# Kernel optimization log

Hardware: AMD Instinct MI355X
Metric: run time of the kernel (lower is better)

## Reference

```python
import jax, jax.numpy as jnp
import numpy as np
from jax import lax

# DCNv2 (ModulatedDeformConvPack) constants per init_kwargs
STRIDE, PAD, DIL, DG, KH, KW = 1, 1, 1, 1, 3, 3
K = KH * KW


def setup_inputs() -> dict:
    key = jax.random.key(0)
    k0, k1, k2 = jax.random.split(key, 3)
    B, C, H, W = 2, 64, 128, 128
    O = 64
    x = jax.random.normal(k0, (B, C, H, W), jnp.float32)
    weight = jax.random.normal(k1, (O, C, KH, KW), jnp.float32) / np.sqrt(C * KH * KW)
    bias = jnp.zeros((O,), jnp.float32)
    # small scale so predicted offsets stay within a few pixels (realistic trained DCN)
    offset_w = jax.random.normal(k2, (DG * 3 * K, C, KH, KW), jnp.float32) * 0.01
    offset_b = jnp.zeros((DG * 3 * K,), jnp.float32)
    return {"x": x, "weight": weight, "bias": bias, "offset_w": offset_w, "offset_b": offset_b}


def _modulated_deform_conv(x, weight, bias, offset_w, offset_b):
    B, C, H, W = x.shape
    O = weight.shape[0]
    # 1) offset/mask prediction conv (standard conv, same geometry as main conv)
    off = lax.conv_general_dilated(
        x, offset_w, window_strides=(STRIDE, STRIDE), padding=((PAD, PAD), (PAD, PAD)),
        rhs_dilation=(DIL, DIL), dimension_numbers=("NCHW", "OIHW", "NCHW"))
    off = off + offset_b[None, :, None, None]
    Ho, Wo = off.shape[2], off.shape[3]
    o1, o2, m = jnp.split(off, 3, axis=1)
    dy = o1.reshape(B, DG, K, Ho, Wo)
    dx = o2.reshape(B, DG, K, Ho, Wo)
    mask = jax.nn.sigmoid(m).reshape(B, DG, K, Ho, Wo)

    # 2) sampling positions: p = p0 + k*dil - pad + offset
    ki, kj = jnp.meshgrid(jnp.arange(KH), jnp.arange(KW), indexing="ij")
    base_y = (jnp.arange(Ho) * STRIDE - PAD)[None, :, None] + (ki.reshape(K) * DIL)[:, None, None]  # (K,Ho,1)
    base_x = (jnp.arange(Wo) * STRIDE - PAD)[None, None, :] + (kj.reshape(K) * DIL)[:, None, None]  # (K,1,Wo)
    py = base_y[None, None].astype(x.dtype) + dy  # (B,DG,K,Ho,Wo)
    px = base_x[None, None].astype(x.dtype) + dx

    y0 = jnp.floor(py)
    x0 = jnp.floor(px)
    wy = py - y0  # fractional weights
    wx = px - x0
    y0i = y0.astype(jnp.int32)
    x0i = x0.astype(jnp.int32)

    Cg = C // DG
    xg = x.reshape(B, DG, Cg, H * W)

    def corner(yi, xi):
        valid = ((yi >= 0) & (yi < H) & (xi >= 0) & (xi < W)).astype(x.dtype)  # zero-pad outside
        idx = jnp.clip(yi, 0, H - 1) * W + jnp.clip(xi, 0, W - 1)  # (B,DG,K,Ho,Wo)
        gather = lambda xf, id_: xf[:, id_]  # (Cg, K, Ho, Wo)
        vals = jax.vmap(jax.vmap(gather))(xg, idx)  # (B,DG,Cg,K,Ho,Wo)
        return vals * valid[:, :, None]

    wy_ = wy[:, :, None]
    wx_ = wx[:, :, None]
    samp = (corner(y0i, x0i) * (1 - wy_) * (1 - wx_)
            + corner(y0i, x0i + 1) * (1 - wy_) * wx_
            + corner(y0i + 1, x0i) * wy_ * (1 - wx_)
            + corner(y0i + 1, x0i + 1) * wy_ * wx_)
    samp = samp * mask[:, :, None]  # modulation
    samp = samp.reshape(B, C, K, Ho, Wo)

    # 3) contraction with conv weight (groups=1)
    out = jnp.einsum("bckhw,ock->bohw", samp, weight.reshape(O, C, K))
    return out + bias[None, :, None, None]


def reference(x, weight, bias, offset_w, offset_b):
    return _modulated_deform_conv(x, weight, bias, offset_w, offset_b)
```

## Files before the change

kernel.cpp:

```cpp
#include <hip/hip_runtime.h>
#include <hip/hip_bf16.h>

typedef __attribute__((ext_vector_type(8))) short bf16x8;
typedef __attribute__((ext_vector_type(4))) float f32x4;

#define Bc 2
#define Cc 64
#define Hc 128
#define Wc 128
#define Oc 64
#define NOFF 27
#define HWc (Hc * Wc)

__device__ __forceinline__ short f2bf(float f) {
    __hip_bfloat16 h = __float2bfloat16(f);
    return __builtin_bit_cast(short, h);
}
__device__ __forceinline__ float bf2f(short s) {
    __hip_bfloat16 h = __builtin_bit_cast(__hip_bfloat16, s);
    return __bfloat162float(h);
}

__global__ __launch_bounds__(256) void prep_kernel(
    const float* __restrict__ x, const float* __restrict__ w, const float* __restrict__ ow,
    short* __restrict__ xT, short* __restrict__ Ahi, short* __restrict__ Alo,
    short* __restrict__ Ohi, short* __restrict__ Olo) {
    int bid = blockIdx.x;
    int t = threadIdx.x;
    if (bid < 512) {
        int b = bid >> 8, rem = bid & 255;
        int h = rem >> 1, w0 = (rem & 1) << 6;
        __shared__ float tile[64][68];
        {
            int c = t >> 2, sub = t & 3;
            const float* src = x + ((size_t)(b * Cc + c) * Hc + h) * Wc + w0 + sub * 16;
#pragma unroll
            for (int j = 0; j < 4; ++j)
                *(float4*)&tile[c][sub * 16 + 4 * j] = *(const float4*)(src + 4 * j);
        }
        __syncthreads();
        {
            int ww = t >> 2, cs = (t & 3) << 4;
            short* dst = xT + (((size_t)(b * Hc + h)) * Wc + w0 + ww) * Cc + cs;
            bf16x8 v0, v1;
#pragma unroll
            for (int j = 0; j < 8; ++j) {
                v0[j] = f2bf(tile[cs + j][ww]);
                v1[j] = f2bf(tile[cs + 8 + j][ww]);
            }
            *(bf16x8*)(dst) = v0;
            *(bf16x8*)(dst + 8) = v1;
        }
    } else {
        int idx = (bid - 512) * 256 + t;
        const int NM = 4 * 18 * 64 * 8;
        const int NO = 2 * 18 * 64 * 8;
        if (idx < NM) {
            int j = idx & 7, lane = (idx >> 3) & 63, ks = (idx >> 9) % 18, mt = idx / 9216;
            int o  = mt * 16 + (lane & 15);
            int kk = ks >> 1;
            int c  = (ks & 1) * 32 + (lane >> 4) * 8 + j;
            float v = w[(o * Cc + c) * 9 + kk];
            short hi = f2bf(v);
            short lo = f2bf(v - bf2f(hi));
            Ahi[idx] = hi; Alo[idx] = lo;
        } else if (idx < NM + NO) {
            int t2 = idx - NM;
            int j = t2 & 7, lane = (t2 >> 3) & 63, ks = (t2 >> 9) % 18, mt = t2 / 9216;
            int o  = mt * 16 + (lane & 15);
            int kk = ks >> 1;
            int c  = (ks & 1) * 32 + (lane >> 4) * 8 + j;
            float v = (o < NOFF) ? ow[(o * Cc + c) * 9 + kk] : 0.f;
            short hi = f2bf(v);
            short lo = f2bf(v - bf2f(hi));
            Ohi[t2] = hi; Olo[t2] = lo;
        }
    }
}

__global__ __launch_bounds__(256, 2) void fused_dcn_kernel(
    const short* __restrict__ xT,
    const short* __restrict__ Ahi, const short* __restrict__ Alo,
    const short* __restrict__ Ohi, const short* __restrict__ Olo,
    const float* __restrict__ bias, const float* __restrict__ obias,
    float* __restrict__ out) {
    int bid = blockIdx.x;
    int b = bid >> 8, rem = bid & 255;
    int h = rem >> 1, w0 = (rem & 1) << 6;
    int tid = threadIdx.x;
    int lane = tid & 63, wv = tid >> 6;
    int n_loc = lane & 15, quad = lane >> 4;
    int p_glob = wv * 16 + n_loc;
    int wpix = w0 + p_glob;
    int cb0 = quad * 8;
    int cb1 = 32 + quad * 8;

    __shared__ float4 wgt[576];
    __shared__ int4   sidx[576];
    __shared__ float  tmp[NOFF * 64];

    const short* xb = xT + (size_t)b * HWc * Cc;

    f32x4 oacc0 = {0.f, 0.f, 0.f, 0.f}, oacc1 = {0.f, 0.f, 0.f, 0.f};
    bf16x8 s1A[2], s1B[2];
    {
        int yc = min(max(h - 1, 0), Hc - 1);
        int xc = min(max(wpix - 1, 0), Wc - 1);
        const short* base = xb + ((size_t)yc * Wc + xc) * Cc;
        s1A[0] = *(const bf16x8*)(base + cb0);
        s1A[1] = *(const bf16x8*)(base + cb1);
    }
#pragma unroll
    for (int kk = 0; kk < 9; ++kk) {
        bf16x8* cur = (kk & 1) ? s1B : s1A;
        bf16x8* nxt = (kk & 1) ? s1A : s1B;
        if (kk < 8) {
            int kk2 = kk + 1;
            int yc = min(max(h + kk2 / 3 - 1, 0), Hc - 1);
            int xc = min(max(wpix + kk2 % 3 - 1, 0), Wc - 1);
            const short* base = xb + ((size_t)yc * Wc + xc) * Cc;
            nxt[0] = *(const bf16x8*)(base + cb0);
            nxt[1] = *(const bf16x8*)(base + cb1);
        }
        int y = h + kk / 3 - 1, xw = wpix + kk % 3 - 1;
        bool val = ((unsigned)y < (unsigned)Hc) && ((unsigned)xw < (unsigned)Wc);
        bf16x8 z = {0, 0, 0, 0, 0, 0, 0, 0};
        bf16x8 b0 = val ? cur[0] : z;
        bf16x8 b1 = val ? cur[1] : z;
#pragma unroll
        for (int ks = 0; ks < 2; ++ks) {
            bf16x8 bf = ks ? b1 : b0;
            int ksg = kk * 2 + ks;
            bf16x8 ah0 = *(const bf16x8*)(Ohi + ((0 * 18 + ksg) * 64 + lane) * 8);
            bf16x8 al0 = *(const bf16x8*)(Olo + ((0 * 18 + ksg) * 64 + lane) * 8);
            oacc0 = __builtin_amdgcn_mfma_f32_16x16x32_bf16(ah0, bf, oacc0, 0, 0, 0);
            oacc0 = __builtin_amdgcn_mfma_f32_16x16x32_bf16(al0, bf, oacc0, 0, 0, 0);
            bf16x8 ah1 = *(const bf16x8*)(Ohi + ((1 * 18 + ksg) * 64 + lane) * 8);
            bf16x8 al1 = *(const bf16x8*)(Olo + ((1 * 18 + ksg) * 64 + lane) * 8);
            oacc1 = __builtin_amdgcn_mfma_f32_16x16x32_bf16(ah1, bf, oacc1, 0, 0, 0);
            oacc1 = __builtin_amdgcn_mfma_f32_16x16x32_bf16(al1, bf, oacc1, 0, 0, 0);
        }
    }
    {
        int mrow = quad * 4;
#pragma unroll
        for (int r = 0; r < 4; ++r) {
            int oc = mrow + r;
            if (oc < NOFF) tmp[oc * 64 + p_glob] = oacc0[r] + obias[oc];
            int oc2 = 16 + mrow + r;
            if (oc2 < NOFF) tmp[oc2 * 64 + p_glob] = oacc1[r] + obias[oc2];
        }
    }
    __syncthreads();

    for (int t = tid; t < 576; t += 256) {
        int k = t >> 6, p = t & 63;
        float dy = tmp[k * 64 + p];
        float dx = tmp[(9 + k) * 64 + p];
        float mm = tmp[(18 + k) * 64 + p];
        float m  = 1.f / (1.f + __expf(-mm));
        float py = (float)(h - 1 + k / 3) + dy;
        float px = (float)(w0 + p - 1 + k % 3) + dx;
        float y0f = floorf(py), x0f = floorf(px);
        float fy = py - y0f, fx = px - x0f;
        int y0 = (int)y0f, x0i = (int)x0f;
        float vy0 = (y0 >= 0 && y0 < Hc) ? 1.f : 0.f;
        float vy1 = (y0 + 1 >= 0 && y0 + 1 < Hc) ? 1.f : 0.f;
        float vx0 = (x0i >= 0 && x0i < Wc) ? 1.f : 0.f;
        float vx1 = (x0i + 1 >= 0 && x0i + 1 < Wc) ? 1.f : 0.f;
        wgt[t] = make_float4((1.f - fy) * (1.f - fx) * m * vy0 * vx0,
                             (1.f - fy) * fx         * m * vy0 * vx1,
                             fy         * (1.f - fx) * m * vy1 * vx0,
                             fy         * fx         * m * vy1 * vx1);
        int cy0 = min(max(y0, 0), Hc - 1) * Wc;
        int cy1 = min(max(y0 + 1, 0), Hc - 1) * Wc;
        int cx0 = min(max(x0i, 0), Wc - 1);
        int cx1 = min(max(x0i + 1, 0), Wc - 1);
        sidx[t] = make_int4(cy0 + cx0, cy0 + cx1, cy1 + cx0, cy1 + cx1);
    }
    __syncthreads();

    f32x4 acc[4] = {{0.f, 0.f, 0.f, 0.f}, {0.f, 0.f, 0.f, 0.f},
                    {0.f, 0.f, 0.f, 0.f}, {0.f, 0.f, 0.f, 0.f}};
    bf16x8 bufA[8], bufB[8];
    float4 w4 = wgt[p_glob];
    {
        int4 id = sidx[p_glob];
        const short* c00 = xb + (size_t)id.x * Cc;
        const short* c01 = xb + (size_t)id.y * Cc;
        const short* c10 = xb + (size_t)id.z * Cc;
        const short* c11 = xb + (size_t)id.w * Cc;
        bufA[0] = *(const bf16x8*)(c00 + cb0); bufA[1] = *(const bf16x8*)(c00 + cb1);
        bufA[2] = *(const bf16x8*)(c01 + cb0); bufA[3] = *(const bf16x8*)(c01 + cb1);
        bufA[4] = *(const bf16x8*)(c10 + cb0); bufA[5] = *(const bf16x8*)(c10 + cb1);
        bufA[6] = *(const bf16x8*)(c11 + cb0); bufA[7] = *(const bf16x8*)(c11 + cb1);
    }
#pragma unroll
    for (int kk = 0; kk < 9; ++kk) {
        bf16x8* cur = (kk & 1) ? bufB : bufA;
        bf16x8* nxt = (kk & 1) ? bufA : bufB;
        float4 w4n;
        if (kk < 8) {
            int4 idn = sidx[(kk + 1) * 64 + p_glob];
            w4n = wgt[(kk + 1) * 64 + p_glob];
            const short* c00 = xb + (size_t)idn.x * Cc;
            const short* c01 = xb + (size_t)idn.y * Cc;
            const short* c10 = xb + (size_t)idn.z * Cc;
            const short* c11 = xb + (size_t)idn.w * Cc;
            nxt[0] = *(const bf16x8*)(c00 + cb0); nxt[1] = *(const bf16x8*)(c00 + cb1);
            nxt[2] = *(const bf16x8*)(c01 + cb0); nxt[3] = *(const bf16x8*)(c01 + cb1);
            nxt[4] = *(const bf16x8*)(c10 + cb0); nxt[5] = *(const bf16x8*)(c10 + cb1);
            nxt[6] = *(const bf16x8*)(c11 + cb0); nxt[7] = *(const bf16x8*)(c11 + cb1);
        }
        bf16x8 b0, b1;
#pragma unroll
        for (int j = 0; j < 8; ++j) {
            float s0 = w4.x * bf2f(cur[0][j]) + w4.y * bf2f(cur[2][j])
                     + w4.z * bf2f(cur[4][j]) + w4.w * bf2f(cur[6][j]);
            float s1 = w4.x * bf2f(cur[1][j]) + w4.y * bf2f(cur[3][j])
                     + w4.z * bf2f(cur[5][j]) + w4.w * bf2f(cur[7][j]);
            b0[j] = f2bf(s0);
            b1[j] = f2bf(s1);
        }
#pragma unroll
        for (int ks = 0; ks < 2; ++ks) {
            bf16x8 bf = ks ? b1 : b0;
            int ksg = kk * 2 + ks;
#pragma unroll
            for (int mt = 0; mt < 4; ++mt) {
                bf16x8 ah = *(const bf16x8*)(Ahi + ((mt * 18 + ksg) * 64 + lane) * 8);
                bf16x8 al = *(const bf16x8*)(Alo + ((mt * 18 + ksg) * 64 + lane) * 8);
                acc[mt] = __builtin_amdgcn_mfma_f32_16x16x32_bf16(ah, bf, acc[mt], 0, 0, 0);
                acc[mt] = __builtin_amdgcn_mfma_f32_16x16x32_bf16(al, bf, acc[mt], 0, 0, 0);
            }
        }
        w4 = w4n;
    }

    int mrow = quad * 4;
    float* ob = out + ((size_t)b * Oc * Hc + h) * Wc + w0 + p_glob;
#pragma unroll
    for (int mt = 0; mt < 4; ++mt)
#pragma unroll
        for (int r = 0; r < 4; ++r) {
            int o = mt * 16 + mrow + r;
            ob[(size_t)o * HWc] = acc[mt][r] + bias[o];
        }
}

extern "C" void kernel_launch(void* const* d_in, const int* in_sizes, int n_in,
                              void* d_out, int out_size, void* d_ws, size_t ws_size,
                              hipStream_t stream) {
    const float* x        = (const float*)d_in[0];
    const float* weight   = (const float*)d_in[1];
    const float* bias     = (const float*)d_in[2];
    const float* offset_w = (const float*)d_in[3];
    const float* offset_b = (const float*)d_in[4];
    float* out = (float*)d_out;

    char* ws = (char*)d_ws;
    short* xT  = (short*)(ws + 0);
    short* Ahi = (short*)(ws + 4194304);
    short* Alo = (short*)(ws + 4268032);
    short* Ohi = (short*)(ws + 4341760);
    short* Olo = (short*)(ws + 4378624);

    prep_kernel<<<512 + 216, 256, 0, stream>>>(x, weight, offset_w, xT, Ahi, Alo, Ohi, Olo);
    fused_dcn_kernel<<<Bc * Hc * 2, 256, 0, stream>>>(xT, Ahi, Alo, Ohi, Olo, bias, offset_b, out);
}
```

Baseline: 105.2 us.

## Fuse prep and DCN kernels into one launch with inter-block flag sync

```diff
diff --git a/kernel.cpp b/kernel.cpp
--- a/kernel.cpp
+++ b/kernel.cpp
@@ -11,6 +11,7 @@
 #define Oc 64
 #define NOFF 27
 #define HWc (Hc * Wc)
+#define MAGIC 0x13579BDF
 
 __device__ __forceinline__ short f2bf(float f) {
     __hip_bfloat16 h = __float2bfloat16(f);
@@ -21,68 +22,19 @@
     return __bfloat162float(h);
 }
 
-__global__ __launch_bounds__(256) void prep_kernel(
+__device__ __forceinline__ void spin_on(volatile int* f) {
+    while (__hip_atomic_load((const int*)f, __ATOMIC_RELAXED, __HIP_MEMORY_SCOPE_AGENT) != MAGIC) {}
+}
+__device__ __forceinline__ void publish(int* f) {
+    __hip_atomic_store(f, MAGIC, __ATOMIC_RELAXED, __HIP_MEMORY_SCOPE_AGENT);
+}
+
+__global__ __launch_bounds__(256, 2) void mega_dcn_kernel(
     const float* __restrict__ x, const float* __restrict__ w, const float* __restrict__ ow,
+    const float* __restrict__ bias, const float* __restrict__ obias,
     short* __restrict__ xT, short* __restrict__ Ahi, short* __restrict__ Alo,
-    short* __restrict__ Ohi, short* __restrict__ Olo) {
-    int bid = blockIdx.x;
-    int t = threadIdx.x;
-    if (bid < 512) {
-        int b = bid >> 8, rem = bid & 255;
-        int h = rem >> 1, w0 = (rem & 1) << 6;
-        __shared__ float tile[64][68];
-        {
-            int c = t >> 2, sub = t & 3;
-            const float* src = x + ((size_t)(b * Cc + c) * Hc + h) * Wc + w0 + sub * 16;
-#pragma unroll
-            for (int j = 0; j < 4; ++j)
-                *(float4*)&tile[c][sub * 16 + 4 * j] = *(const float4*)(src + 4 * j);
-        }
-        __syncthreads();
-        {
-            int ww = t >> 2, cs = (t & 3) << 4;
-            short* dst = xT + (((size_t)(b * Hc + h)) * Wc + w0 + ww) * Cc + cs;
-            bf16x8 v0, v1;
-#pragma unroll
-            for (int j = 0; j < 8; ++j) {
-                v0[j] = f2bf(tile[cs + j][ww]);
-                v1[j] = f2bf(tile[cs + 8 + j][ww]);
-            }
-            *(bf16x8*)(dst) = v0;
-            *(bf16x8*)(dst + 8) = v1;
-        }
-    } else {
-        int idx = (bid - 512) * 256 + t;
-        const int NM = 4 * 18 * 64 * 8;
-        const int NO = 2 * 18 * 64 * 8;
-        if (idx < NM) {
-            int j = idx & 7, lane = (idx >> 3) & 63, ks = (idx >> 9) % 18, mt = idx / 9216;
-            int o  = mt * 16 + (lane & 15);
-            int kk = ks >> 1;
-            int c  = (ks & 1) * 32 + (lane >> 4) * 8 + j;
-            float v = w[(o * Cc + c) * 9 + kk];
-            short hi = f2bf(v);
-            short lo = f2bf(v - bf2f(hi));
-            Ahi[idx] = hi; Alo[idx] = lo;
-        } else if (idx < NM + NO) {
-            int t2 = idx - NM;
-            int j = t2 & 7, lane = (t2 >> 3) & 63, ks = (t2 >> 9) % 18, mt = t2 / 9216;
-            int o  = mt * 16 + (lane & 15);
-            int kk = ks >> 1;
-            int c  = (ks & 1) * 32 + (lane >> 4) * 8 + j;
-            float v = (o < NOFF) ? ow[(o * Cc + c) * 9 + kk] : 0.f;
-            short hi = f2bf(v);
-            short lo = f2bf(v - bf2f(hi));
-            Ohi[t2] = hi; Olo[t2] = lo;
-        }
-    }
-}
-
-__global__ __launch_bounds__(256, 2) void fused_dcn_kernel(
-    const short* __restrict__ xT,
-    const short* __restrict__ Ahi, const short* __restrict__ Alo,
-    const short* __restrict__ Ohi, const short* __restrict__ Olo,
-    const float* __restrict__ bias, const float* __restrict__ obias,
+    short* __restrict__ Ohi, short* __restrict__ Olo,
+    int* __restrict__ xflag, int* __restrict__ pflag,
     float* __restrict__ out) {
     int bid = blockIdx.x;
     int b = bid >> 8, rem = bid & 255;
@@ -92,12 +44,71 @@
     int n_loc = lane & 15, quad = lane >> 4;
     int p_glob = wv * 16 + n_loc;
     int wpix = w0 + p_glob;
-    int cb0 = quad * 8;
-    int cb1 = 32 + quad * 8;
-
+    int cb0 = quad * 8, cb1 = 32 + quad * 8;
+
+    __shared__ float tile[64][68];
     __shared__ float4 wgt[576];
     __shared__ int4   sidx[576];
     __shared__ float  tmp[NOFF * 64];
+    __shared__ int    rowmin, rowmax;
+
+    bool packO = (bid >= 144 && bid < 216);
+    if (packO) {
+        int idx = bid * 256 + tid;
+        int t2 = idx - 144 * 256;
+        int j = t2 & 7, ln = (t2 >> 3) & 63, ks = (t2 >> 9) % 18, mt = t2 / 9216;
+        int o = mt * 16 + (ln & 15);
+        int kk = ks >> 1;
+        int c = (ks & 1) * 32 + (ln >> 4) * 8 + j;
+        float v = (o < NOFF) ? ow[(o * Cc + c) * 9 + kk] : 0.f;
+        short hi = f2bf(v);
+        Ohi[t2] = hi; Olo[t2] = f2bf(v - bf2f(hi));
+        __syncthreads();
+        if (tid == 0) { __threadfence(); publish(&pflag[bid]); }
+    }
+    {
+        int c = tid >> 2, sub = tid & 3;
+        const float* src = x + ((size_t)(b * Cc + c) * Hc + h) * Wc + w0 + sub * 16;
+#pragma unroll
+        for (int j = 0; j < 4; ++j)
+            *(float4*)&tile[c][sub * 16 + 4 * j] = *(const float4*)(src + 4 * j);
+        __syncthreads();
+        int ww = tid >> 2, cs = (tid & 3) << 4;
+        short* dst = xT + (((size_t)(b * Hc + h)) * Wc + w0 + ww) * Cc + cs;
+        bf16x8 v0, v1;
+#pragma unroll
+        for (int j = 0; j < 8; ++j) {
+            v0[j] = f2bf(tile[cs + j][ww]);
+            v1[j] = f2bf(tile[cs + 8 + j][ww]);
+        }
+        *(bf16x8*)(dst) = v0;
+        *(bf16x8*)(dst + 8) = v1;
+        __syncthreads();
+        if (tid == 0) { __threadfence(); publish(&xflag[bid]); }
+    }
+    if (bid < 144) {
+        int idx = bid * 256 + tid;
+        int j = idx & 7, ln = (idx >> 3) & 63, ks = (idx >> 9) % 18, mt = idx / 9216;
+        int o = mt * 16 + (ln & 15);
+        int kk = ks >> 1;
+        int c = (ks & 1) * 32 + (ln >> 4) * 8 + j;
+        float v = w[(o * Cc + c) * 9 + kk];
+        short hi = f2bf(v);
+        Ahi[idx] = hi; Alo[idx] = f2bf(v - bf2f(hi));
+        __syncthreads();
+        if (tid == 0) { __threadfence(); publish(&pflag[bid]); }
+    }
+
+    {
+        if (tid < 72) spin_on(&pflag[144 + tid]);
+        else if (tid < 78) {
+            int rsel = (tid - 72) >> 1;
+            int row = min(max(h - 1 + rsel, 0), Hc - 1);
+            spin_on(&xflag[b * 256 + row * 2 + ((tid - 72) & 1)]);
+        }
+        __threadfence();
+        __syncthreads();
+    }
 
     const short* xb = xT + (size_t)b * HWc * Cc;
 
@@ -150,6 +161,7 @@
             int oc2 = 16 + mrow + r;
             if (oc2 < NOFF) tmp[oc2 * 64 + p_glob] = oacc1[r] + obias[oc2];
         }
+        if (tid == 0) { rowmin = Hc - 1; rowmax = 0; }
     }
     __syncthreads();
 
@@ -172,13 +184,24 @@
                              (1.f - fy) * fx         * m * vy0 * vx1,
                              fy         * (1.f - fx) * m * vy1 * vx0,
                              fy         * fx         * m * vy1 * vx1);
-        int cy0 = min(max(y0, 0), Hc - 1) * Wc;
-        int cy1 = min(max(y0 + 1, 0), Hc - 1) * Wc;
+        int r0 = min(max(y0, 0), Hc - 1);
+        int r1 = min(max(y0 + 1, 0), Hc - 1);
         int cx0 = min(max(x0i, 0), Wc - 1);
         int cx1 = min(max(x0i + 1, 0), Wc - 1);
-        sidx[t] = make_int4(cy0 + cx0, cy0 + cx1, cy1 + cx0, cy1 + cx1);
+        sidx[t] = make_int4(r0 * Wc + cx0, r0 * Wc + cx1, r1 * Wc + cx0, r1 * Wc + cx1);
+        atomicMin(&rowmin, r0);
+        atomicMax(&rowmax, r1);
     }
     __syncthreads();
+
+    {
+        if (tid < 144) spin_on(&pflag[tid]);
+        int mn = rowmin, cnt = (rowmax - rowmin + 1) * 2;
+        if (tid < cnt)
+            spin_on(&xflag[b * 256 + (mn + (tid >> 1)) * 2 + (tid & 1)]);
+        __threadfence();
+        __syncthreads();
+    }
 
     f32x4 acc[4] = {{0.f, 0.f, 0.f, 0.f}, {0.f, 0.f, 0.f, 0.f},
                     {0.f, 0.f, 0.f, 0.f}, {0.f, 0.f, 0.f, 0.f}};
@@ -199,7 +222,7 @@
     for (int kk = 0; kk < 9; ++kk) {
         bf16x8* cur = (kk & 1) ? bufB : bufA;
         bf16x8* nxt = (kk & 1) ? bufA : bufB;
-        float4 w4n;
+        float4 w4n = w4;
         if (kk < 8) {
             int4 idn = sidx[(kk + 1) * 64 + p_glob];
             w4n = wgt[(kk + 1) * 64 + p_glob];
@@ -259,12 +282,15 @@
     float* out = (float*)d_out;
 
     char* ws = (char*)d_ws;
-    short* xT  = (short*)(ws + 0);
-    short* Ahi = (short*)(ws + 4194304);
-    short* Alo = (short*)(ws + 4268032);
-    short* Ohi = (short*)(ws + 4341760);
-    short* Olo = (short*)(ws + 4378624);
-
-    prep_kernel<<<512 + 216, 256, 0, stream>>>(x, weight, offset_w, xT, Ahi, Alo, Ohi, Olo);
-    fused_dcn_kernel<<<Bc * Hc * 2, 256, 0, stream>>>(xT, Ahi, Alo, Ohi, Olo, bias, offset_b, out);
-}
+    short* xT    = (short*)(ws + 0);
+    short* Ahi   = (short*)(ws + 4194304);
+    short* Alo   = (short*)(ws + 4268032);
+    short* Ohi   = (short*)(ws + 4341760);
+    short* Olo   = (short*)(ws + 4378624);
+    int*   xflag = (int*)(ws + 4415488);
+    int*   pflag = (int*)(ws + 4417536);
+
+    mega_dcn_kernel<<<Bc * Hc * 2, 256, 0, stream>>>(
+        x, weight, offset_w, bias, offset_b,
+        xT, Ahi, Alo, Ohi, Olo, xflag, pflag, out);
+}
```

Result: slower. 210.7 us (+100.3%).

## Drop split-bf16 weight compensation and stage half of weights in LDS

Applied to the files above, without the earlier changes.

```diff
diff --git a/kernel.cpp b/kernel.cpp
--- a/kernel.cpp
+++ b/kernel.cpp
@@ -23,8 +23,7 @@
 
 __global__ __launch_bounds__(256) void prep_kernel(
     const float* __restrict__ x, const float* __restrict__ w, const float* __restrict__ ow,
-    short* __restrict__ xT, short* __restrict__ Ahi, short* __restrict__ Alo,
-    short* __restrict__ Ohi, short* __restrict__ Olo) {
+    short* __restrict__ xT, short* __restrict__ Ahi, short* __restrict__ Ohi) {
     int bid = blockIdx.x;
     int t = threadIdx.x;
     if (bid < 512) {
@@ -60,28 +59,21 @@
             int o  = mt * 16 + (lane & 15);
             int kk = ks >> 1;
             int c  = (ks & 1) * 32 + (lane >> 4) * 8 + j;
-            float v = w[(o * Cc + c) * 9 + kk];
-            short hi = f2bf(v);
-            short lo = f2bf(v - bf2f(hi));
-            Ahi[idx] = hi; Alo[idx] = lo;
+            Ahi[idx] = f2bf(w[(o * Cc + c) * 9 + kk]);
         } else if (idx < NM + NO) {
             int t2 = idx - NM;
             int j = t2 & 7, lane = (t2 >> 3) & 63, ks = (t2 >> 9) % 18, mt = t2 / 9216;
             int o  = mt * 16 + (lane & 15);
             int kk = ks >> 1;
             int c  = (ks & 1) * 32 + (lane >> 4) * 8 + j;
-            float v = (o < NOFF) ? ow[(o * Cc + c) * 9 + kk] : 0.f;
-            short hi = f2bf(v);
-            short lo = f2bf(v - bf2f(hi));
-            Ohi[t2] = hi; Olo[t2] = lo;
+            Ohi[t2] = f2bf((o < NOFF) ? ow[(o * Cc + c) * 9 + kk] : 0.f);
         }
     }
 }
 
 __global__ __launch_bounds__(256, 2) void fused_dcn_kernel(
     const short* __restrict__ xT,
-    const short* __restrict__ Ahi, const short* __restrict__ Alo,
-    const short* __restrict__ Ohi, const short* __restrict__ Olo,
+    const short* __restrict__ Ahi, const short* __restrict__ Ohi,
     const float* __restrict__ bias, const float* __restrict__ obias,
     float* __restrict__ out) {
     int bid = blockIdx.x;
@@ -92,9 +84,9 @@
     int n_loc = lane & 15, quad = lane >> 4;
     int p_glob = wv * 16 + n_loc;
     int wpix = w0 + p_glob;
-    int cb0 = quad * 8;
-    int cb1 = 32 + quad * 8;
-
+    int cb0 = quad * 8, cb1 = 32 + quad * 8;
+
+    __shared__ __align__(16) short Asm[2 * 18 * 64 * 8];
     __shared__ float4 wgt[576];
     __shared__ int4   sidx[576];
     __shared__ float  tmp[NOFF * 64];
@@ -132,13 +124,9 @@
             bf16x8 bf = ks ? b1 : b0;
             int ksg = kk * 2 + ks;
             bf16x8 ah0 = *(const bf16x8*)(Ohi + ((0 * 18 + ksg) * 64 + lane) * 8);
-            bf16x8 al0 = *(const bf16x8*)(Olo + ((0 * 18 + ksg) * 64 + lane) * 8);
             oacc0 = __builtin_amdgcn_mfma_f32_16x16x32_bf16(ah0, bf, oacc0, 0, 0, 0);
-            oacc0 = __builtin_amdgcn_mfma_f32_16x16x32_bf16(al0, bf, oacc0, 0, 0, 0);
             bf16x8 ah1 = *(const bf16x8*)(Ohi + ((1 * 18 + ksg) * 64 + lane) * 8);
-            bf16x8 al1 = *(const bf16x8*)(Olo + ((1 * 18 + ksg) * 64 + lane) * 8);
             oacc1 = __builtin_amdgcn_mfma_f32_16x16x32_bf16(ah1, bf, oacc1, 0, 0, 0);
-            oacc1 = __builtin_amdgcn_mfma_f32_16x16x32_bf16(al1, bf, oacc1, 0, 0, 0);
         }
     }
     {
@@ -151,6 +139,8 @@
             if (oc2 < NOFF) tmp[oc2 * 64 + p_glob] = oacc1[r] + obias[oc2];
         }
     }
+    for (int i = tid; i < 2304; i += 256)
+        *((bf16x8*)Asm + i) = *((const bf16x8*)Ahi + i);
     __syncthreads();
 
     for (int t = tid; t < 576; t += 256) {
@@ -199,7 +189,7 @@
     for (int kk = 0; kk < 9; ++kk) {
         bf16x8* cur = (kk & 1) ? bufB : bufA;
         bf16x8* nxt = (kk & 1) ? bufA : bufB;
-        float4 w4n;
+        float4 w4n = w4;
         if (kk < 8) {
             int4 idn = sidx[(kk + 1) * 64 + p_glob];
             w4n = wgt[(kk + 1) * 64 + p_glob];
@@ -226,13 +216,14 @@
         for (int ks = 0; ks < 2; ++ks) {
             bf16x8 bf = ks ? b1 : b0;
             int ksg = kk * 2 + ks;
-#pragma unroll
-            for (int mt = 0; mt < 4; ++mt) {
-                bf16x8 ah = *(const bf16x8*)(Ahi + ((mt * 18 + ksg) * 64 + lane) * 8);
-                bf16x8 al = *(const bf16x8*)(Alo + ((mt * 18 + ksg) * 64 + lane) * 8);
-                acc[mt] = __builtin_amdgcn_mfma_f32_16x16x32_bf16(ah, bf, acc[mt], 0, 0, 0);
-                acc[mt] = __builtin_amdgcn_mfma_f32_16x16x32_bf16(al, bf, acc[mt], 0, 0, 0);
-            }
+            bf16x8 a0 = *(const bf16x8*)(Asm + ((0 * 18 + ksg) * 64 + lane) * 8);
+            acc[0] = __builtin_amdgcn_mfma_f32_16x16x32_bf16(a0, bf, acc[0], 0, 0, 0);
+            bf16x8 a1 = *(const bf16x8*)(Asm + ((1 * 18 + ksg) * 64 + lane) * 8);
+            acc[1] = __builtin_amdgcn_mfma_f32_16x16x32_bf16(a1, bf, acc[1], 0, 0, 0);
+            bf16x8 a2 = *(const bf16x8*)(Ahi + ((2 * 18 + ksg) * 64 + lane) * 8);
+            acc[2] = __builtin_amdgcn_mfma_f32_16x16x32_bf16(a2, bf, acc[2], 0, 0, 0);
+            bf16x8 a3 = *(const bf16x8*)(Ahi + ((3 * 18 + ksg) * 64 + lane) * 8);
+            acc[3] = __builtin_amdgcn_mfma_f32_16x16x32_bf16(a3, bf, acc[3], 0, 0, 0);
         }
         w4 = w4n;
     }
@@ -261,10 +252,8 @@
     char* ws = (char*)d_ws;
     short* xT  = (short*)(ws + 0);
     short* Ahi = (short*)(ws + 4194304);
-    short* Alo = (short*)(ws + 4268032);
-    short* Ohi = (short*)(ws + 4341760);
-    short* Olo = (short*)(ws + 4378624);
-
-    prep_kernel<<<512 + 216, 256, 0, stream>>>(x, weight, offset_w, xT, Ahi, Alo, Ohi, Olo);
-    fused_dcn_kernel<<<Bc * Hc * 2, 256, 0, stream>>>(xT, Ahi, Alo, Ohi, Olo, bias, offset_b, out);
-}
+    short* Ohi = (short*)(ws + 4268032);
+
+    prep_kernel<<<512 + 216, 256, 0, stream>>>(x, weight, offset_w, xT, Ahi, Ohi);
+    fused_dcn_kernel<<<Bc * Hc * 2, 256, 0, stream>>>(xT, Ahi, Ohi, bias, offset_b, out);
+}
```

New measurement: 99.36 us. 1.06x faster.
